# Performance work log

Hardware: AMD Instinct MI355X
Metric: run time of the kernel (lower is better)

## Reference

```python
import jax, jax.numpy as jnp
import numpy as np

# dims: B graphs, NE entity nodes, NR relation nodes, N total nodes, D=hsz, H heads, P prop steps
B, NE, NR, D, H, P = 4, 1536, 512, 128, 4, 2
N = NE + NR
DH = D // H
RV = 500  # relation vocab
EPS = 1e-5


def setup_inputs() -> dict:
    key = jax.random.key(0)
    ks = jax.random.split(key, 20)
    s = 0.02
    inp = {
        "vents": jax.random.normal(ks[0], (B, NE, D), dtype=jnp.float32),
        "rels": jax.random.randint(ks[1], (B, NR), 0, RV),
        "adj": jax.random.randint(ks[2], (B, N, N), 0, 2, dtype=jnp.int32),
        "entlens": jnp.full((B,), NE, dtype=jnp.int32),
        "renc_w": jax.random.normal(ks[3], (RV, D), dtype=jnp.float32) * s,
        # per-prop-step attention params (torch Linear stored as [in, out])
        "Wq": jax.random.normal(ks[4], (P, D, D)) * s,
        "bq": jnp.zeros((P, D)),
        "Wk": jax.random.normal(ks[5], (P, D, D)) * s,
        "bk": jnp.zeros((P, D)),
        "Wv": jax.random.normal(ks[6], (P, D, D)) * s,
        "bv": jnp.zeros((P, D)),
        "Wo": jax.random.normal(ks[7], (P, D, D)) * s,
        "bo": jnp.zeros((P, D)),
        # Block FFN hsz -> 4*hsz -> hsz
        "l1_w": jax.random.normal(ks[8], (P, D, 4 * D)) * s,
        "l1_b": jnp.zeros((P, 4 * D)),
        "l2_w": jax.random.normal(ks[9], (P, 4 * D, D)) * s,
        "l2_b": jnp.zeros((P, D)),
        # ln_1 is used for BOTH norms in Block (faithful to original bug)
        "ln_g": jnp.ones((P, D)),
        "ln_b": jnp.zeros((P, D)),
        # PReLU per-channel slope, torch default 0.25
        "prelu_a": jnp.full((P, 4 * D), 0.25, dtype=jnp.float32),
    }
    return inp


def _ln(x, g, b):
    m = x.mean(-1, keepdims=True)
    v = ((x - m) ** 2).mean(-1, keepdims=True)
    return (x - m) / jnp.sqrt(v + EPS) * g + b


def reference(vents, rels, adj, entlens, renc_w,
              Wq, bq, Wk, bk, Wv, bv, Wo, bo,
              l1_w, l1_b, l2_w, l2_b, ln_g, ln_b, prelu_a):
    # vgraph_i = cat(vents[i][:entlens[i]], renc(rels[i])) -> all graphs same size, batched
    vgraph = jnp.concatenate([vents, renc_w[rels]], axis=1)  # [B, N, D]
    mask = (adj == 0)  # [B, N, N] True = masked out
    scale = 1.0 / np.sqrt(DH).astype(np.float32)
    for p in range(P):
        q_in = vgraph
        kv_in = jax.lax.stop_gradient(vgraph)  # dense path: ngraph is detached
        Q = (q_in @ Wq[p] + bq[p]).reshape(B, N, H, DH)
        K = (kv_in @ Wk[p] + bk[p]).reshape(B, N, H, DH)
        V = (kv_in @ Wv[p] + bv[p]).reshape(B, N, H, DH)
        scores = jnp.einsum('bihd,bjhd->bhij', Q, K) * scale  # [B, H, N, N]
        scores = jnp.where(mask[:, None, :, :], -1e9, scores)
        A = jax.nn.softmax(scores, axis=-1)
        O = jnp.einsum('bhij,bjhd->bihd', A, V).reshape(B, N, D) @ Wo[p] + bo[p]
        # Block feed-forward (dropout = identity in eval)
        t = _ln(O, ln_g[p], ln_b[p])
        h1 = t @ l1_w[p] + l1_b[p]
        h1 = jnp.where(h1 >= 0, h1, prelu_a[p] * h1)  # PReLU
        q2 = h1 @ l2_w[p] + l2_b[p]
        vgraph = _ln(q2 + t, ln_g[p], ln_b[p])
    glob = vgraph[jnp.arange(B), entlens]  # vgraph[entlens[i]] per graph -> [B, D]
    gents = vgraph  # all graphs same length, no padding needed -> [B, N, D]
    emask = jnp.ones((B, N), dtype=bool)  # arange(N) <= N is all True
    return glob, gents, emask
```

## Files before the change

### kernel.cpp

```cpp
#include <hip/hip_runtime.h>
#include <hip/hip_bf16.h>

typedef __bf16 bf16;
typedef __bf16 bf16x4 __attribute__((ext_vector_type(4)));
typedef __bf16 bf16x8 __attribute__((ext_vector_type(8)));
typedef float f32x4 __attribute__((ext_vector_type(4)));
typedef float f32x16 __attribute__((ext_vector_type(16)));

#define B_ 4
#define NE_ 1536
#define NR_ 512
#define N_ 2048
#define D_ 128
#define H_ 4
#define DH_ 32
#define P_ 2
#define M_ (B_*N_)
#define NW_ (N_/32)
#define SK_ 4
#define KCH_ (N_/SK_)
#define NIT_ (KCH_/64)

__device__ __forceinline__ f32x4 mfma16(bf16x8 a, bf16x8 b, f32x4 c) {
    return __builtin_amdgcn_mfma_f32_16x16x32_bf16(a, b, c, 0, 0, 0);
}
__device__ __forceinline__ f32x16 mfma32(bf16x8 a, bf16x8 b, f32x16 c) {
    return __builtin_amdgcn_mfma_f32_32x32x16_bf16(a, b, c, 0, 0, 0);
}
__device__ __forceinline__ unsigned cvtpk(float lo, float hi) {
    unsigned r;
    asm("v_cvt_pk_bf16_f32 %0, %1, %2" : "=v"(r) : "v"(lo), "v"(hi));
    return r;
}
__device__ __forceinline__ void swap32(unsigned& a, unsigned& b) {
    asm("v_permlane32_swap_b32 %0, %1" : "+v"(a), "+v"(b));
}
__device__ __forceinline__ void gload16(const void* g, void* l) {
    __builtin_amdgcn_global_load_lds(
        (const __attribute__((address_space(1))) void*)g,
        (__attribute__((address_space(3))) void*)l, 16, 0, 0);
}

#define VGN_ (B_*N_*D_)
#define MKN_ (B_*N_*NW_)
#define PPER_ (3*16384 + 16384 + 65536 + 65536 + 384)
#define PRN_ (P_*PPER_)
__global__ void k_prep(const float* __restrict__ vents, const int* __restrict__ rels,
                       const float* __restrict__ renc, const int* __restrict__ adj,
                       const float* __restrict__ Wq, const float* __restrict__ Wk,
                       const float* __restrict__ Wv, const float* __restrict__ Wo,
                       const float* __restrict__ l1w, const float* __restrict__ l2w,
                       const float* __restrict__ bq, const float* __restrict__ bk,
                       const float* __restrict__ bv,
                       bf16* __restrict__ vb, unsigned int* __restrict__ mw,
                       bf16* __restrict__ wqkvT, float* __restrict__ bqkv,
                       bf16* __restrict__ woT, bf16* __restrict__ l1T,
                       bf16* __restrict__ l2T) {
    const float SC = 0.25503330560513437f;
    int idx = blockIdx.x * 256 + threadIdx.x;
    if (idx < VGN_) {
        int d = idx & (D_ - 1);
        int n = (idx >> 7) & (N_ - 1);
        int b = idx >> 18;
        float v;
        if (n < NE_) v = vents[((size_t)(b * NE_ + n)) * D_ + d];
        else         v = renc[(size_t)rels[b * NR_ + (n - NE_)] * D_ + d];
        vb[idx] = (bf16)v;
        return;
    }
    idx -= VGN_;
    if (idx < MKN_) {
        const int4* a = (const int4*)(adj + (size_t)idx * 32);
        unsigned int w = 0;
#pragma unroll
        for (int q = 0; q < 8; ++q) {
            int4 t = a[q];
            w |= (t.x != 0 ? 1u : 0u) << (q * 4 + 0);
            w |= (t.y != 0 ? 1u : 0u) << (q * 4 + 1);
            w |= (t.z != 0 ? 1u : 0u) << (q * 4 + 2);
            w |= (t.w != 0 ? 1u : 0u) << (q * 4 + 3);
        }
        mw[idx] = w;
        return;
    }
    idx -= MKN_;
    if (idx >= PRN_) return;
    int p = idx / PPER_;
    int r = idx % PPER_;
    if (r < 3 * 16384) {
        int which = r / 16384, e = r % 16384;
        int o = e >> 7, i = e & 127;
        const float* W = which == 0 ? Wq : (which == 1 ? Wk : Wv);
        float v = W[(size_t)(p * 128 + i) * 128 + o];
        if (which == 0) v *= SC;
        wqkvT[(size_t)(p * 384 + which * 128 + o) * 128 + i] = (bf16)v;
    } else if ((r -= 3 * 16384) < 16384) {
        int o = r >> 7, i = r & 127;
        woT[(size_t)(p * 128 + o) * 128 + i] = (bf16)Wo[(size_t)(p * 128 + i) * 128 + o];
    } else if ((r -= 16384) < 65536) {
        int o = r >> 7, i = r & 127;
        l1T[(size_t)(p * 512 + o) * 128 + i] = (bf16)l1w[(size_t)(p * 128 + i) * 512 + o];
    } else if ((r -= 65536) < 65536) {
        int o = r >> 9, i = r & 511;
        l2T[(size_t)(p * 128 + o) * 512 + i] = (bf16)l2w[(size_t)(p * 512 + i) * 128 + o];
    } else {
        r -= 65536;
        float v = r < 128 ? bq[p * 128 + r] * SC
                          : (r < 256 ? bk[p * 128 + r - 128] : bv[p * 128 + r - 256]);
        bqkv[p * 384 + r] = v;
    }
}

__global__ __launch_bounds__(256) void k_qkv(
        const bf16* __restrict__ X, const bf16* __restrict__ WT,
        const float* __restrict__ bias,
        bf16* __restrict__ Qout, bf16* __restrict__ Kout,
        bf16* __restrict__ VTout) {
    int lane = threadIdx.x & 63, wid = threadIdx.x >> 6;
    int wr = wid >> 1, wc = wid & 1;
    int m0 = blockIdx.x * 64 + wr * 32;
    int n0 = blockIdx.y * 64 + wc * 32;
    int lr = lane & 15, lg = lane >> 4;
    f32x4 acc[2][2];
#pragma unroll
    for (int mi = 0; mi < 2; ++mi)
#pragma unroll
        for (int ni = 0; ni < 2; ++ni)
            acc[mi][ni] = f32x4{0.f, 0.f, 0.f, 0.f};

    for (int k0 = 0; k0 < 128; k0 += 32) {
        bf16x8 a[2], bb[2];
#pragma unroll
        for (int mi = 0; mi < 2; ++mi)
            a[mi] = *(const bf16x8*)(X + (size_t)(m0 + mi * 16 + lr) * 128 + k0 + lg * 8);
#pragma unroll
        for (int ni = 0; ni < 2; ++ni)
            bb[ni] = *(const bf16x8*)(WT + (size_t)(n0 + ni * 16 + lr) * 128 + k0 + lg * 8);
#pragma unroll
        for (int mi = 0; mi < 2; ++mi)
#pragma unroll
            for (int ni = 0; ni < 2; ++ni)
                acc[mi][ni] = mfma16(a[mi], bb[ni], acc[mi][ni]);
    }
#pragma unroll
    for (int mi = 0; mi < 2; ++mi) {
#pragma unroll
        for (int ni = 0; ni < 2; ++ni) {
            int col = n0 + ni * 16 + lr;
            float bs = bias[col];
            int rowb = m0 + mi * 16 + lg * 4;
            if (col < 128) {
#pragma unroll
                for (int r = 0; r < 4; ++r)
                    Qout[(size_t)(rowb + r) * D_ + col] = (bf16)(acc[mi][ni][r] + bs);
            } else if (col < 256) {
#pragma unroll
                for (int r = 0; r < 4; ++r)
                    Kout[(size_t)(rowb + r) * D_ + (col - 128)] = (bf16)(acc[mi][ni][r] + bs);
            } else {
                int d = col - 256, h = d >> 5, dh = d & 31;
                int b = rowb >> 11, nn = rowb & (N_ - 1);
                bf16x4 pk;
#pragma unroll
                for (int r = 0; r < 4; ++r) pk[r] = (bf16)(acc[mi][ni][r] + bs);
                *(bf16x4*)(VTout + ((size_t)(b * H_ + h) * DH_ + dh) * N_ + nn) = pk;
            }
        }
    }
}

__global__ __launch_bounds__(256) void k_attn(
    const bf16* __restrict__ Q, const bf16* __restrict__ Kt,
    const bf16* __restrict__ VT, const unsigned int* __restrict__ mw,
    bf16* __restrict__ partO, float* __restrict__ partML) {
    __shared__ __align__(16) char kbuf[4][4096];
    __shared__ __align__(16) char vbuf[4][4096];
    int wid = threadIdx.x >> 6;
    int lane = threadIdx.x & 63;
    int ql = lane & 31, hf = lane >> 5;
    int hw = blockIdx.x + 16 * blockIdx.y + 256 * blockIdx.z;
    int work = (hw & 7) * 128 + (hw >> 3);
    int qx = work & 15;
    int bh = (work >> 4) & 15;
    int kc = work >> 8;
    int b = bh >> 2, h = bh & 3;
    int qg = qx * 128 + wid * 32 + ql;
    const size_t bnD = (size_t)b * N_ * D_;

    const bf16* qp = Q + bnD + (size_t)qg * D_ + h * 32 + hf * 8;
    bf16x8 qf0 = *(const bf16x8*)(qp);
    bf16x8 qf1 = *(const bf16x8*)(qp + 16);

    const uint4* mp4 = (const uint4*)(mw + ((size_t)b * N_ + qg) * NW_ + kc * (KCH_ / 32));
    uint4 mk0 = mp4[0], mk1 = mp4[1], mk2 = mp4[2], mk3 = mp4[3];
    unsigned mword[16] = {mk0.x, mk0.y, mk0.z, mk0.w, mk1.x, mk1.y, mk1.z, mk1.w,
                          mk2.x, mk2.y, mk2.z, mk2.w, mk3.x, mk3.y, mk3.z, mk3.w};

    const char* kg = (const char*)(Kt + bnD + (size_t)(kc * KCH_) * D_) + h * 64;
    const char* vg = (const char*)(VT + (size_t)(bh * DH_) * N_ + kc * KCH_);

    f32x16 of;
#pragma unroll
    for (int i = 0; i < 16; ++i) of[i] = 0.f;
    const f32x16 zero16 = of;
    float lsum = 0.f;

#define STAGE(bufi, it) do {                                                   \
        int k0s = (it) * 64;                                                   \
        gload16(kg + (size_t)(k0s + lane) * 256 + wid * 16,                    \
                kbuf[bufi] + wid * 1024);                                      \
        gload16(vg + ((size_t)(lane & 31) * N_ + k0s) * 2 +                    \
                    (2 * wid + (lane >> 5)) * 16,                              \
                vbuf[bufi] + wid * 1024);                                      \
    } while (0)

    STAGE(0, 0);
    STAGE(1, 1);

#pragma unroll
    for (int it = 0; it < NIT_; ++it) {
        int cur = it & 3;
        if (it + 2 < NIT_) STAGE((it + 2) & 3, it + 2);
        if (it < NIT_ - 2)       asm volatile("s_waitcnt vmcnt(4)" ::: "memory");
        else if (it == NIT_ - 2) asm volatile("s_waitcnt vmcnt(2)" ::: "memory");
        else                     asm volatile("s_waitcnt vmcnt(0)" ::: "memory");
        __builtin_amdgcn_s_barrier();
        __builtin_amdgcn_sched_barrier(0);

#pragma unroll
        for (int kb = 0; kb < 2; ++kb) {
            bf16x8 kf0 = *(const bf16x8*)(kbuf[cur] + hf * 1024 + (kb * 32 + ql) * 16);
            bf16x8 kf1 = *(const bf16x8*)(kbuf[cur] + 2048 + hf * 1024 + (kb * 32 + ql) * 16);
            f32x16 s = mfma32(kf0, qf0, zero16);
            s = mfma32(kf1, qf1, s);

            unsigned wsh = mword[it * 2 + kb] >> (hf * 4);
            float p[16];
#pragma unroll
            for (int r = 0; r < 16; ++r) {
                int bitp = (r & 3) + 8 * (r >> 2);
                float e = __builtin_amdgcn_exp2f(s[r]);
                p[r] = ((wsh >> bitp) & 1u) ? e : 0.f;
            }
            float a0 = (p[0] + p[1]) + (p[2] + p[3]);
            float a1 = (p[4] + p[5]) + (p[6] + p[7]);
            float a2 = (p[8] + p[9]) + (p[10] + p[11]);
            float a3 = (p[12] + p[13]) + (p[14] + p[15]);
            lsum += (a0 + a1) + (a2 + a3);

            unsigned lo0 = cvtpk(p[0], p[1]),   hi0 = cvtpk(p[2], p[3]);
            unsigned lo1 = cvtpk(p[4], p[5]),   hi1 = cvtpk(p[6], p[7]);
            unsigned lo2 = cvtpk(p[8], p[9]),   hi2 = cvtpk(p[10], p[11]);
            unsigned lo3 = cvtpk(p[12], p[13]), hi3 = cvtpk(p[14], p[15]);
            swap32(lo0, lo1); swap32(hi0, hi1);
            swap32(lo2, lo3); swap32(hi2, hi3);
            union { unsigned u[4]; bf16x8 v; } f0, f1;
            f0.u[0] = lo0; f0.u[1] = hi0; f0.u[2] = lo1; f0.u[3] = hi1;
            f1.u[0] = lo2; f1.u[1] = hi2; f1.u[2] = lo3; f1.u[3] = hi3;

            bf16x8 va = *(const bf16x8*)(vbuf[cur] + ((kb * 2 + 0) * 2 + hf) * 512 + ql * 16);
            bf16x8 vb2 = *(const bf16x8*)(vbuf[cur] + ((kb * 2 + 1) * 2 + hf) * 512 + ql * 16);
            __builtin_amdgcn_s_setprio(1);
            of = mfma32(va, f0.v, of);
            of = mfma32(vb2, f1.v, of);
            __builtin_amdgcn_s_setprio(0);
        }
    }
#undef STAGE

    lsum += __shfl_xor(lsum, 32, 64);
    size_t pb = ((size_t)(kc * 16 + bh) * N_ + qg) * 32;
#pragma unroll
    for (int g = 0; g < 4; ++g) {
        union { unsigned u[2]; bf16x4 v; } pk;
        pk.u[0] = cvtpk(of[4 * g + 0], of[4 * g + 1]);
        pk.u[1] = cvtpk(of[4 * g + 2], of[4 * g + 3]);
        *(bf16x4*)(partO + pb + 8 * g + 4 * hf) = pk.v;
    }
    if (lane < 32)
        partML[(size_t)(kc * 16 + bh) * N_ + qg] = lsum;
}

template <bool LAST>
__global__ __launch_bounds__(512) void k_ffn(
        const bf16* __restrict__ partO, const float* __restrict__ partML,
        const bf16* __restrict__ woT, const float* __restrict__ bo,
        const bf16* __restrict__ l1T, const float* __restrict__ l1b,
        const float* __restrict__ pra,
        const bf16* __restrict__ l2T, const float* __restrict__ l2b,
        const float* __restrict__ lng, const float* __restrict__ lnb,
        const bf16* __restrict__ wqkvT2, const float* __restrict__ bqkv2,
        const int* __restrict__ entl, float* __restrict__ gout,
        bf16* __restrict__ Qout, bf16* __restrict__ Kout,
        bf16* __restrict__ VTout) {
    __shared__ __align__(16) char Obuf[16 * 256];
    __shared__ __align__(16) char Tbuf[16 * 256];
    __shared__ __align__(16) char Hbuf[16 * 1024];
    __shared__ float lst[8][16][2];
    int t = threadIdx.x;
    int lane = t & 63, wid = t >> 6;
    int lr = lane & 15, lg = lane >> 4;
    int m0 = blockIdx.x * 16;

    {
        int i = t >> 5, u = t & 31;
        int r = m0 + i, b = r >> 11, q = r & (N_ - 1);
        int h = u >> 3, dh4 = u & 7;
        int bh = b * 4 + h;
        float L = 0.f;
        f32x4 o = {0.f, 0.f, 0.f, 0.f};
#pragma unroll
        for (int kc = 0; kc < SK_; ++kc) {
            size_t base = (size_t)(kc * 16 + bh) * N_ + q;
            L += partML[base];
            bf16x4 pv = *(const bf16x4*)(partO + base * 32 + dh4 * 4);
#pragma unroll
            for (int j = 0; j < 4; ++j) o[j] += (float)pv[j];
        }
        float rL = 1.f / L;
        bf16x4 pk;
#pragma unroll
        for (int j = 0; j < 4; ++j) pk[j] = (bf16)(o[j] * rL);
        *(bf16x4*)(Obuf + i * 256 + ((u * 8) ^ ((i & 7) << 4))) = pk;
    }
    __syncthreads();

    float tvx[4];
    {
        int n0 = wid * 16;
        f32x4 acc = {0.f, 0.f, 0.f, 0.f};
#pragma unroll
        for (int k0 = 0; k0 < 128; k0 += 32) {
            bf16x8 a = *(const bf16x8*)(Obuf + lr * 256 + (((k0 + lg * 8) * 2) ^ ((lr & 7) << 4)));
            bf16x8 bb = *(const bf16x8*)(woT + (size_t)(n0 + lr) * 128 + k0 + lg * 8);
            acc = mfma16(a, bb, acc);
        }
        int col = n0 + lr;
        float bs = bo[col];
#pragma unroll
        for (int r2 = 0; r2 < 4; ++r2) tvx[r2] = acc[r2] + bs;
#pragma unroll
        for (int r2 = 0; r2 < 4; ++r2) {
            float sv = tvx[r2], qv = tvx[r2] * tvx[r2];
#pragma unroll
            for (int msk = 1; msk < 16; msk <<= 1) {
                sv += __shfl_xor(sv, msk, 64);
                qv += __shfl_xor(qv, msk, 64);
            }
            if (lr == 0) { lst[wid][lg * 4 + r2][0] = sv; lst[wid][lg * 4 + r2][1] = qv; }
        }
        __syncthreads();
#pragma unroll
        for (int r2 = 0; r2 < 4; ++r2) {
            int row = lg * 4 + r2;
            float S = 0.f, Q2 = 0.f;
#pragma unroll
            for (int w2 = 0; w2 < 8; ++w2) { S += lst[w2][row][0]; Q2 += lst[w2][row][1]; }
            float mean = S * (1.f / 128.f);
            float var = Q2 * (1.f / 128.f) - mean * mean;
            float rstd = rsqrtf(var + 1e-5f);
            float o = (tvx[r2] - mean) * rstd * lng[col] + lnb[col];
            tvx[r2] = o;
            *(bf16*)(Tbuf + row * 256 + ((col * 2) ^ ((row & 7) << 4))) = (bf16)o;
        }
    }
    __syncthreads();

    {
        int n0 = wid * 64;
        f32x4 acc[4];
#pragma unroll
        for (int ni = 0; ni < 4; ++ni) acc[ni] = f32x4{0.f, 0.f, 0.f, 0.f};
#pragma unroll
        for (int k0 = 0; k0 < 128; k0 += 32) {
            bf16x8 a = *(const bf16x8*)(Tbuf + lr * 256 + (((k0 + lg * 8) * 2) ^ ((lr & 7) << 4)));
#pragma unroll
            for (int ni = 0; ni < 4; ++ni) {
                bf16x8 bb = *(const bf16x8*)(l1T + (size_t)(n0 + ni * 16 + lr) * 128 + k0 + lg * 8);
                acc[ni] = mfma16(a, bb, acc[ni]);
            }
        }
#pragma unroll
        for (int ni = 0; ni < 4; ++ni) {
            int col = n0 + ni * 16 + lr;
            float bs = l1b[col], sl = pra[col];
#pragma unroll
            for (int r2 = 0; r2 < 4; ++r2) {
                int row = lg * 4 + r2;
                float v = acc[ni][r2] + bs;
                v = v >= 0.f ? v : sl * v;
                *(bf16*)(Hbuf + row * 1024 + ((col * 2) ^ ((row & 7) << 4))) = (bf16)v;
            }
        }
    }
    __syncthreads();

    {
        int n0 = wid * 16;
        f32x4 acc = {0.f, 0.f, 0.f, 0.f};
#pragma unroll
        for (int k0 = 0; k0 < 512; k0 += 32) {
            bf16x8 a = *(const bf16x8*)(Hbuf + lr * 1024 + (((k0 + lg * 8) * 2) ^ ((lr & 7) << 4)));
            bf16x8 bb = *(const bf16x8*)(l2T + (size_t)(n0 + lr) * 512 + k0 + lg * 8);
            acc = mfma16(a, bb, acc);
        }
        int col = n0 + lr;
        float bs = l2b[col];
        float vx[4];
#pragma unroll
        for (int r2 = 0; r2 < 4; ++r2)
            vx[r2] = acc[r2] + bs + tvx[r2];
        __syncthreads();
#pragma unroll
        for (int r2 = 0; r2 < 4; ++r2) {
            float sv = vx[r2], qv = vx[r2] * vx[r2];
#pragma unroll
            for (int msk = 1; msk < 16; msk <<= 1) {
                sv += __shfl_xor(sv, msk, 64);
                qv += __shfl_xor(qv, msk, 64);
            }
            if (lr == 0) { lst[wid][lg * 4 + r2][0] = sv; lst[wid][lg * 4 + r2][1] = qv; }
        }
        __syncthreads();
#pragma unroll
        for (int r2 = 0; r2 < 4; ++r2) {
            int row = lg * 4 + r2;
            float S = 0.f, Q2 = 0.f;
#pragma unroll
            for (int w2 = 0; w2 < 8; ++w2) { S += lst[w2][row][0]; Q2 += lst[w2][row][1]; }
            float mean = S * (1.f / 128.f);
            float var = Q2 * (1.f / 128.f) - mean * mean;
            float rstd = rsqrtf(var + 1e-5f);
            float o = (vx[r2] - mean) * rstd * lng[col] + lnb[col];
            size_t rowg = (size_t)(m0 + row);
            if (LAST) {
                float* gents = gout + 512;
                gents[rowg * 128 + col] = o;
                int b = (int)(rowg >> 11);
                if ((int)(rowg & (N_ - 1)) == entl[b])
                    gout[b * 128 + col] = o;
            } else {
                *(bf16*)(Obuf + row * 256 + ((col * 2) ^ ((row & 7) << 4))) = (bf16)o;
            }
        }
        if (LAST && t < 16)
            gout[512 + (size_t)M_ * 128 + m0 + t] = 1.0f;
    }

    if (!LAST) {
        __syncthreads();
        int n0q = wid * 48;
        f32x4 acc[3];
#pragma unroll
        for (int ni = 0; ni < 3; ++ni) acc[ni] = f32x4{0.f, 0.f, 0.f, 0.f};
#pragma unroll
        for (int k0 = 0; k0 < 128; k0 += 32) {
            bf16x8 a = *(const bf16x8*)(Obuf + lr * 256 + (((k0 + lg * 8) * 2) ^ ((lr & 7) << 4)));
#pragma unroll
            for (int ni = 0; ni < 3; ++ni) {
                bf16x8 bb = *(const bf16x8*)(wqkvT2 + (size_t)(n0q + ni * 16 + lr) * 128 + k0 + lg * 8);
                acc[ni] = mfma16(a, bb, acc[ni]);
            }
        }
#pragma unroll
        for (int ni = 0; ni < 3; ++ni) {
            int col = n0q + ni * 16 + lr;
            float bs = bqkv2[col];
            int rowb = m0 + lg * 4;
            if (col < 128) {
#pragma unroll
                for (int r = 0; r < 4; ++r)
                    Qout[(size_t)(rowb + r) * D_ + col] = (bf16)(acc[ni][r] + bs);
            } else if (col < 256) {
#pragma unroll
                for (int r = 0; r < 4; ++r)
                    Kout[(size_t)(rowb + r) * D_ + (col - 128)] = (bf16)(acc[ni][r] + bs);
            } else {
                int d = col - 256, h = d >> 5, dh = d & 31;
                int b = rowb >> 11, nn = rowb & (N_ - 1);
                bf16x4 pk;
#pragma unroll
                for (int r = 0; r < 4; ++r) pk[r] = (bf16)(acc[ni][r] + bs);
                *(bf16x4*)(VTout + ((size_t)(b * H_ + h) * DH_ + dh) * N_ + nn) = pk;
            }
        }
    }
}

extern "C" void kernel_launch(void* const* d_in, const int* in_sizes, int n_in,
                              void* d_out, int out_size, void* d_ws, size_t ws_size,
                              hipStream_t stream) {
    const float* vents = (const float*)d_in[0];
    const int*   rels  = (const int*)d_in[1];
    const int*   adj   = (const int*)d_in[2];
    const int*   entl  = (const int*)d_in[3];
    const float* renc  = (const float*)d_in[4];
    const float* Wq = (const float*)d_in[5];
    const float* bq = (const float*)d_in[6];
    const float* Wk = (const float*)d_in[7];
    const float* bk = (const float*)d_in[8];
    const float* Wv = (const float*)d_in[9];
    const float* bv = (const float*)d_in[10];
    const float* Wo = (const float*)d_in[11];
    const float* bo = (const float*)d_in[12];
    const float* l1w = (const float*)d_in[13];
    const float* l1b = (const float*)d_in[14];
    const float* l2w = (const float*)d_in[15];
    const float* l2b = (const float*)d_in[16];
    const float* lng = (const float*)d_in[17];
    const float* lnb = (const float*)d_in[18];
    const float* pra = (const float*)d_in[19];

    char* w = (char*)d_ws;
    auto alloc = [&](size_t bytes) { char* r = w; w += (bytes + 255) & ~(size_t)255; return r; };
    bf16*  vb    = (bf16*)alloc((size_t)M_ * D_ * 2);
    unsigned int* mw = (unsigned int*)alloc((size_t)B_ * N_ * NW_ * 4);
    bf16*  wqkvT = (bf16*)alloc((size_t)P_ * 384 * 128 * 2);
    float* bqkv  = (float*)alloc((size_t)P_ * 384 * 4);
    bf16*  woT   = (bf16*)alloc((size_t)P_ * 128 * 128 * 2);
    bf16*  l1T   = (bf16*)alloc((size_t)P_ * 512 * 128 * 2);
    bf16*  l2T   = (bf16*)alloc((size_t)P_ * 128 * 512 * 2);
    bf16*  Qb    = (bf16*)alloc((size_t)M_ * D_ * 2);
    bf16*  Kb    = (bf16*)alloc((size_t)M_ * D_ * 2);
    bf16*  VTb   = (bf16*)alloc((size_t)M_ * D_ * 2);
    bf16*  partO  = (bf16*)alloc((size_t)SK_ * 16 * N_ * 32 * 2);
    float* partML = (float*)alloc((size_t)SK_ * 16 * N_ * 4);
    float* gout  = (float*)d_out;

    const int PRTOT = VGN_ + MKN_ + PRN_;
    k_prep<<<(PRTOT + 255) / 256, 256, 0, stream>>>(
        vents, rels, renc, adj, Wq, Wk, Wv, Wo, l1w, l2w, bq, bk, bv,
        vb, mw, wqkvT, bqkv, woT, l1T, l2T);
    k_qkv<<<dim3(M_ / 64, 384 / 64), 256, 0, stream>>>(
        vb, wqkvT, bqkv, Qb, Kb, VTb);
    k_attn<<<dim3(16, 16, SK_), 256, 0, stream>>>(Qb, Kb, VTb, mw, partO, partML);
    k_ffn<false><<<M_ / 16, 512, 0, stream>>>(
        partO, partML, woT, bo, l1T, l1b, pra, l2T, l2b, lng, lnb,
        wqkvT + (size_t)384 * 128, bqkv + 384, entl, nullptr, Qb, Kb, VTb);
    k_attn<<<dim3(16, 16, SK_), 256, 0, stream>>>(Qb, Kb, VTb, mw, partO, partML);
    k_ffn<true><<<M_ / 16, 512, 0, stream>>>(
        partO, partML, woT + (size_t)128 * 128, bo + 128,
        l1T + (size_t)512 * 128, l1b + 512, pra + 512,
        l2T + (size_t)128 * 512, l2b + 128, lng + 128, lnb + 128,
        wqkvT, bqkv, entl, gout, Qb, Kb, VTb);
}
```

Before: 131.8 us.

## Stage attention mask words in LDS and stop unrolling the key loop

The attention kernel now loads each block's mask bitwords cooperatively into a shared-memory buffer. Each iteration reads only the two words it needs, instead of holding sixteen mask words per lane in registers. The key-chunk loop is no longer fully unrolled. Both changes aim to cut register pressure and code size so occupancy can rise. The XCD-aware block-index remapping is also dropped in favour of direct blockIdx mapping, which may change L2 locality across dies.

```diff
diff --git a/kernel.cpp b/kernel.cpp
--- a/kernel.cpp
+++ b/kernel.cpp
@@ -175,14 +175,13 @@
     bf16* __restrict__ partO, float* __restrict__ partML) {
     __shared__ __align__(16) char kbuf[4][4096];
     __shared__ __align__(16) char vbuf[4][4096];
+    __shared__ __align__(16) unsigned mbuf[128][16];
     int wid = threadIdx.x >> 6;
     int lane = threadIdx.x & 63;
     int ql = lane & 31, hf = lane >> 5;
-    int hw = blockIdx.x + 16 * blockIdx.y + 256 * blockIdx.z;
-    int work = (hw & 7) * 128 + (hw >> 3);
-    int qx = work & 15;
-    int bh = (work >> 4) & 15;
-    int kc = work >> 8;
+    int qx = blockIdx.x;
+    int bh = blockIdx.y;
+    int kc = blockIdx.z;
     int b = bh >> 2, h = bh & 3;
     int qg = qx * 128 + wid * 32 + ql;
     const size_t bnD = (size_t)b * N_ * D_;
@@ -191,10 +190,15 @@
     bf16x8 qf0 = *(const bf16x8*)(qp);
     bf16x8 qf1 = *(const bf16x8*)(qp + 16);
 
-    const uint4* mp4 = (const uint4*)(mw + ((size_t)b * N_ + qg) * NW_ + kc * (KCH_ / 32));
-    uint4 mk0 = mp4[0], mk1 = mp4[1], mk2 = mp4[2], mk3 = mp4[3];
-    unsigned mword[16] = {mk0.x, mk0.y, mk0.z, mk0.w, mk1.x, mk1.y, mk1.z, mk1.w,
-                          mk2.x, mk2.y, mk2.z, mk2.w, mk3.x, mk3.y, mk3.z, mk3.w};
+#pragma unroll
+    for (int j = 0; j < 2; ++j) {
+        int u = threadIdx.x + 256 * j;
+        int row = u >> 2, sub = u & 3;
+        uint4 mv = *(const uint4*)(mw + ((size_t)b * N_ + qx * 128 + row) * NW_
+                                      + kc * (KCH_ / 32) + sub * 4);
+        *(uint4*)(&mbuf[row][sub * 4]) = mv;
+    }
+    asm volatile("s_waitcnt lgkmcnt(0)" ::: "memory");
 
     const char* kg = (const char*)(Kt + bnD + (size_t)(kc * KCH_) * D_) + h * 64;
     const char* vg = (const char*)(VT + (size_t)(bh * DH_) * N_ + kc * KCH_);
@@ -204,6 +208,7 @@
     for (int i = 0; i < 16; ++i) of[i] = 0.f;
     const f32x16 zero16 = of;
     float lsum = 0.f;
+    int mrow = wid * 32 + ql;
 
 #define STAGE(bufi, it) do {                                                   \
         int k0s = (it) * 64;                                                   \
@@ -217,9 +222,10 @@
     STAGE(0, 0);
     STAGE(1, 1);
 
-#pragma unroll
+#pragma unroll 1
     for (int it = 0; it < NIT_; ++it) {
-        int cur = it & 3;
+        const char* kb_ = kbuf[it & 3];
+        const char* vb_ = vbuf[it & 3];
         if (it + 2 < NIT_) STAGE((it + 2) & 3, it + 2);
         if (it < NIT_ - 2)       asm volatile("s_waitcnt vmcnt(4)" ::: "memory");
         else if (it == NIT_ - 2) asm volatile("s_waitcnt vmcnt(2)" ::: "memory");
@@ -227,14 +233,17 @@
         __builtin_amdgcn_s_barrier();
         __builtin_amdgcn_sched_barrier(0);
 
+        unsigned long long mword2 = *(const unsigned long long*)(&mbuf[mrow][it * 2]);
+        unsigned mw0 = (unsigned)mword2, mw1 = (unsigned)(mword2 >> 32);
+
 #pragma unroll
         for (int kb = 0; kb < 2; ++kb) {
-            bf16x8 kf0 = *(const bf16x8*)(kbuf[cur] + hf * 1024 + (kb * 32 + ql) * 16);
-            bf16x8 kf1 = *(const bf16x8*)(kbuf[cur] + 2048 + hf * 1024 + (kb * 32 + ql) * 16);
+            bf16x8 kf0 = *(const bf16x8*)(kb_ + hf * 1024 + (kb * 32 + ql) * 16);
+            bf16x8 kf1 = *(const bf16x8*)(kb_ + 2048 + hf * 1024 + (kb * 32 + ql) * 16);
             f32x16 s = mfma32(kf0, qf0, zero16);
             s = mfma32(kf1, qf1, s);
 
-            unsigned wsh = mword[it * 2 + kb] >> (hf * 4);
+            unsigned wsh = (kb ? mw1 : mw0) >> (hf * 4);
             float p[16];
 #pragma unroll
             for (int r = 0; r < 16; ++r) {
@@ -258,8 +267,8 @@
             f0.u[0] = lo0; f0.u[1] = hi0; f0.u[2] = lo1; f0.u[3] = hi1;
             f1.u[0] = lo2; f1.u[1] = hi2; f1.u[2] = lo3; f1.u[3] = hi3;
 
-            bf16x8 va = *(const bf16x8*)(vbuf[cur] + ((kb * 2 + 0) * 2 + hf) * 512 + ql * 16);
-            bf16x8 vb2 = *(const bf16x8*)(vbuf[cur] + ((kb * 2 + 1) * 2 + hf) * 512 + ql * 16);
+            bf16x8 va = *(const bf16x8*)(vb_ + ((kb * 2 + 0) * 2 + hf) * 512 + ql * 16);
+            bf16x8 vb2 = *(const bf16x8*)(vb_ + ((kb * 2 + 1) * 2 + hf) * 512 + ql * 16);
             __builtin_amdgcn_s_setprio(1);
             of = mfma32(va, f0.v, of);
             of = mfma32(vb2, f1.v, of);
```

New measurement: 131.0 us. About the same (-0.6%).
